# Kernel tuning notes

Hardware: AMD Instinct MI355X
Metric: run time of the kernel (lower is better)

The kernel has to match this reference:

```python
import jax, jax.numpy as jnp
import numpy as np

D_EMB = 64
N_HEADS = 8
D_K = D_EMB // N_HEADS


def setup_inputs() -> dict:
    key = jax.random.key(0)
    ks = jax.random.split(key, 7)
    B, N = 4, 512
    s = 0.02
    return {
        "n": jax.random.normal(ks[0], (B, N, D_EMB), jnp.float32),
        "e": jax.random.normal(ks[1], (B, N, N, D_EMB), jnp.float32),
        # weights stored as (in, out); torch Linear applies x @ W.T
        "W_qkv": jax.random.normal(ks[2], (D_EMB, 3 * D_EMB), jnp.float32) * s,
        "O_n": jax.random.normal(ks[3], (D_EMB, D_EMB), jnp.float32) * s,
        "W_g": jax.random.normal(ks[4], (D_EMB, N_HEADS), jnp.float32) * s,
        "W_e": jax.random.normal(ks[5], (D_EMB, N_HEADS), jnp.float32) * s,
        "O_e": jax.random.normal(ks[6], (N_HEADS, D_EMB), jnp.float32) * s,
    }


def reference(n, e, W_qkv, O_n, W_g, W_e, O_e):
    B, N, _ = n.shape
    H, dk = N_HEADS, D_K
    # QKV projection -> [B, H, N, dk] each
    qkv = (n @ W_qkv).reshape(B, N, 3, H, dk)
    Q = jnp.transpose(qkv[:, :, 0], (0, 2, 1, 3))
    K = jnp.transpose(qkv[:, :, 1], (0, 2, 1, 3))
    V = jnp.transpose(qkv[:, :, 2], (0, 2, 1, 3))
    # per-head edge bias E and gate G: [B, H, N, N]
    E = jnp.transpose(e @ W_e, (0, 3, 1, 2))
    G = jax.nn.sigmoid(jnp.transpose(e @ W_g, (0, 3, 1, 2)))
    dynamic_centrality = jnp.log1p(G.sum(-1))  # [B, H, N]
    # scaled, clamped attention scores plus edge bias
    A_raw = jnp.einsum("bhnd,bhmd->bhnm", Q, K) * (dk ** -0.5)
    A_raw = jnp.clip(A_raw, -5.0, 5.0)
    _E = A_raw + E  # pre-softmax scores, reused for edge output
    A = jax.nn.softmax(_E, axis=-1)
    _V = jnp.einsum("bhnm,bhmd->bhnd", A, V)
    _V = _V * dynamic_centrality[..., None]  # centrality rescale
    n_out = jnp.transpose(_V, (0, 2, 1, 3)).reshape(B, N, H * dk) @ O_n
    e_out = jnp.transpose(_E, (0, 2, 3, 1)) @ O_e  # [B, N, N, d_emb]
    return (n_out, e_out)
```

## Files before the change

kernel.cpp:

```cpp
#include <hip/hip_runtime.h>

#define NN 512
#define SCALE 0.35355339059327373f
#define SMAX 6.0f

typedef short bf16x8 __attribute__((ext_vector_type(8)));
typedef float f32x4 __attribute__((ext_vector_type(4)));

static __device__ __forceinline__ unsigned short bhi16(float x) {
    return (unsigned short)(__float_as_uint(x) >> 16);
}
static __device__ __forceinline__ float btrunc(float x) {
    return __uint_as_float(__float_as_uint(x) & 0xFFFF0000u);
}
static __device__ __forceinline__ unsigned short blo16(float x) {
    return (unsigned short)(__float_as_uint(x - btrunc(x)) >> 16);
}

__global__ __launch_bounds__(64) void qkv_proj(const float* __restrict__ nin,
                                               const float* __restrict__ Wqkv,
                                               float* __restrict__ qkv,
                                               unsigned short* __restrict__ kbf) {
    const int r = blockIdx.x;
    const int j = threadIdx.x;
    const float* nr = nin + (size_t)r * 64;
    float a0 = 0.f, a1 = 0.f, a2 = 0.f;
#pragma unroll
    for (int d = 0; d < 64; ++d) {
        const float nv = nr[d];
        const float* wr = Wqkv + d * 192;
        a0 = fmaf(nv, wr[j], a0);
        a1 = fmaf(nv, wr[64 + j], a1);
        a2 = fmaf(nv, wr[128 + j], a2);
    }
    float* o = qkv + (size_t)r * 192;
    o[j] = a0; o[64 + j] = a1; o[128 + j] = a2;
    kbf[(size_t)r * 64 + j] = bhi16(a1);
}

__device__ __forceinline__ void gload16f(const float* g, float* l) {
    __builtin_amdgcn_global_load_lds(
        (const __attribute__((address_space(1))) unsigned int*)(g),
        (__attribute__((address_space(3))) unsigned int*)(l), 16, 0, 0);
}
__device__ __forceinline__ void gload16u(const unsigned short* g, unsigned short* l) {
    __builtin_amdgcn_global_load_lds(
        (const __attribute__((address_space(1))) unsigned int*)(g),
        (__attribute__((address_space(3))) unsigned int*)(l), 16, 0, 0);
}
#define WAITV(N) asm volatile("s_waitcnt vmcnt(" #N ")" ::: "memory")
#define BARRIER() __builtin_amdgcn_s_barrier()

__global__ __launch_bounds__(256, 2) void edge_mfma5(
    const float* __restrict__ e,
    const float* __restrict__ qkv,
    const unsigned short* __restrict__ kbf,
    const float* __restrict__ We,
    const float* __restrict__ Wg,
    const float* __restrict__ Oe,
    float* __restrict__ e_out,
    float* __restrict__ pvw,
    float* __restrict__ dngs)
{
    __shared__ float ebuf[4][2][16][64];
    __shared__ unsigned short kbl[4][2][16][64];
    __shared__ float Wl[1024];
    __shared__ float Qlds[64];
    __shared__ float Oelds[512];
    __shared__ float E_lds[4][32][8];
    __shared__ float red[256];
    __shared__ float wdn[4][8], wgs[4][8];

    const int t = threadIdx.x, w = t >> 6, l = t & 63;
    const int a2 = l >> 4, m16 = l & 15;
    const int bid = blockIdx.x;
    const int wg = (bid & 7) * 1024 + (bid >> 3);
    const int bn = wg >> 2, chunk = wg & 3;
    const int b = bn >> 9;
    const int rowc = chunk * 128 + w * 32;
    const float* __restrict__ Qp = qkv + (size_t)bn * 192;
    const float* __restrict__ ebase = e + (size_t)bn * 32768;
    float* __restrict__ eob = e_out + (size_t)bn * 32768;

    {
        const float* wsrc = (w < 2) ? (We + w * 256) : (Wg + (w - 2) * 256);
        gload16f(wsrc + l * 4, &Wl[w * 256]);
        if (l < 16) gload16f(Qp + l * 4, &Qlds[0]);
        if (l < 32) gload16f(Oe + w * 128 + l * 4, &Oelds[w * 128]);
    }
#pragma unroll
    for (int s = 0; s < 2; ++s) {
#pragma unroll
        for (int i_ = 0; i_ < 4; ++i_) {
            const int lrow = i_ * 4 + (l >> 4);
            gload16f(ebase + (size_t)(rowc + s * 16 + lrow) * 64 + (((l & 15) ^ lrow) * 4),
                     &ebuf[w][s][i_ * 4][0]);
        }
#pragma unroll
        for (int i_ = 0; i_ < 2; ++i_) {
            const int r8 = i_ * 8 + (l >> 3);
            gload16u(kbf + (size_t)(b * NN + rowc + s * 16 + r8) * 64 + (((l & 7) ^ (r8 & 7)) * 8),
                     &kbl[w][s][i_ * 8][0]);
        }
    }

    WAITV(12);
    BARRIER();

    const int colbase = (m16 < 8) ? m16 : (504 + m16);
    bf16x8 WfB[4], WcB[2], QdB[2];
#pragma unroll
    for (int blk = 0; blk < 4; ++blk) {
#pragma unroll
        for (int jj = 0; jj < 4; ++jj) {
            const int d = blk * 16 + a2 * 4 + jj;
            const short h = (short)bhi16(Wl[d * 8 + colbase]);
            WfB[blk][2 * jj] = h;
            WfB[blk][2 * jj + 1] = h;
        }
    }
#pragma unroll
    for (int c = 0; c < 2; ++c) {
        const int head = c * 4 + a2;
#pragma unroll
        for (int j = 0; j < 8; ++j) {
            const int d = c * 32 + a2 * 8 + j;
            WcB[c][j] = (short)blo16(Wl[d * 8 + colbase]);
            QdB[c][j] = (m16 == head) ? (short)bhi16(Qlds[d]) : (short)0;
        }
    }
    float dn = 0.f, gs = 0.f;

#define SLAB(s, WN) do {                                                         \
        WAITV(WN);                                                               \
        f32x4 c1 = {0.f, 0.f, 0.f, 0.f}, c2 = {0.f, 0.f, 0.f, 0.f};             \
        _Pragma("unroll")                                                        \
        for (int blk = 0; blk < 4; ++blk) {                                      \
            const float4 ev = *(const float4*)&ebuf[w][s][m16]                   \
                                  [(((blk * 4 + a2) ^ m16) * 4)];                \
            bf16x8 af;                                                           \
            af[0] = (short)bhi16(ev.x); af[1] = (short)blo16(ev.x);              \
            af[2] = (short)bhi16(ev.y); af[3] = (short)blo16(ev.y);              \
            af[4] = (short)bhi16(ev.z); af[5] = (short)blo16(ev.z);              \
            af[6] = (short)bhi16(ev.w); af[7] = (short)blo16(ev.w);              \
            c1 = __builtin_amdgcn_mfma_f32_16x16x32_bf16(af, WfB[blk], c1, 0, 0, 0); \
        }                                                                        \
        _Pragma("unroll")                                                        \
        for (int c = 0; c < 2; ++c) {                                            \
            const int g0 = c * 8 + a2 * 2;                                       \
            const float4 e0 = *(const float4*)&ebuf[w][s][m16][((g0 ^ m16) * 4)]; \
            const float4 e1 = *(const float4*)&ebuf[w][s][m16][(((g0 + 1) ^ m16) * 4)]; \
            bf16x8 ac;                                                           \
            ac[0] = (short)bhi16(e0.x); ac[1] = (short)bhi16(e0.y);              \
            ac[2] = (short)bhi16(e0.z); ac[3] = (short)bhi16(e0.w);              \
            ac[4] = (short)bhi16(e1.x); ac[5] = (short)bhi16(e1.y);              \
            ac[6] = (short)bhi16(e1.z); ac[7] = (short)bhi16(e1.w);              \
            c1 = __builtin_amdgcn_mfma_f32_16x16x32_bf16(ac, WcB[c], c1, 0, 0, 0); \
            const bf16x8 kf = *(const bf16x8*)&kbl[w][s][m16]                    \
                                  [(((c * 4 + a2) ^ (m16 & 7)) * 8)];            \
            c2 = __builtin_amdgcn_mfma_f32_16x16x32_bf16(kf, QdB[c], c2, 0, 0, 0); \
        }                                                                        \
        if (m16 < 8) {                                                           \
            _Pragma("unroll")                                                    \
            for (int r = 0; r < 4; ++r) {                                        \
                const float E_ = fminf(fmaxf(c2[r] * SCALE, -5.f), 5.f) + c1[r]; \
                dn += __expf(E_ - SMAX);                                         \
                E_lds[w][(s) * 16 + a2 * 4 + r][m16] = E_;                       \
            }                                                                    \
        } else {                                                                 \
            _Pragma("unroll")                                                    \
            for (int r = 0; r < 4; ++r) gs += 1.f / (1.f + __expf(-c1[r]));      \
        } } while (0)

    SLAB(0, 6);
    SLAB(1, 0);

    dn += __shfl_xor(dn, 16, 64); dn += __shfl_xor(dn, 32, 64);
    gs += __shfl_xor(gs, 16, 64); gs += __shfl_xor(gs, 32, 64);
    if (a2 == 0 && m16 < 8) wdn[w][m16] = dn;
    if (a2 == 0 && m16 >= 8) wgs[w][m16 - 8] = gs;

    {
        const int k = l & 7, hh = (l >> 3) & 7;
        const float* vb = qkv + (size_t)(b * NN + rowc) * 192 + 128 + hh * 8 + k;
        float acc = 0.f;
#pragma unroll 8
        for (int i = 0; i < 32; ++i) {
            const float p = __expf(E_lds[w][i][hh] - SMAX);
            acc = fmaf(p, vb[(size_t)i * 192], acc);
        }
        red[t] = acc;
    }
    __syncthreads();
    if (t < 64)
        pvw[(size_t)wg * 64 + t] = red[t] + red[64 + t] + red[128 + t] + red[192 + t];
    if (t < 8)
        dngs[(size_t)wg * 16 + t] = wdn[0][t] + wdn[1][t] + wdn[2][t] + wdn[3][t];
    else if (t < 16)
        dngs[(size_t)wg * 16 + t] = wgs[0][t - 8] + wgs[1][t - 8] + wgs[2][t - 8] + wgs[3][t - 8];

    {
        const int j4 = l & 15, mr = l >> 4;
        float oc[8][4];
#pragma unroll
        for (int h = 0; h < 8; ++h) {
            const float4 v = *(const float4*)&Oelds[h * 64 + j4 * 4];
            oc[h][0] = v.x; oc[h][1] = v.y; oc[h][2] = v.z; oc[h][3] = v.w;
        }
#pragma unroll 2
        for (int p = 0; p < 8; ++p) {
            const int mloc = p * 4 + mr;
            const float* er = &E_lds[w][mloc][0];
            const float4 ra = *reinterpret_cast<const float4*>(er);
            const float4 rb = *reinterpret_cast<const float4*>(er + 4);
            float o0 = ra.x * oc[0][0], o1 = ra.x * oc[0][1], o2 = ra.x * oc[0][2], o3 = ra.x * oc[0][3];
            o0 = fmaf(ra.y, oc[1][0], o0); o1 = fmaf(ra.y, oc[1][1], o1); o2 = fmaf(ra.y, oc[1][2], o2); o3 = fmaf(ra.y, oc[1][3], o3);
            o0 = fmaf(ra.z, oc[2][0], o0); o1 = fmaf(ra.z, oc[2][1], o1); o2 = fmaf(ra.z, oc[2][2], o2); o3 = fmaf(ra.z, oc[2][3], o3);
            o0 = fmaf(ra.w, oc[3][0], o0); o1 = fmaf(ra.w, oc[3][1], o1); o2 = fmaf(ra.w, oc[3][2], o2); o3 = fmaf(ra.w, oc[3][3], o3);
            o0 = fmaf(rb.x, oc[4][0], o0); o1 = fmaf(rb.x, oc[4][1], o1); o2 = fmaf(rb.x, oc[4][2], o2); o3 = fmaf(rb.x, oc[4][3], o3);
            o0 = fmaf(rb.y, oc[5][0], o0); o1 = fmaf(rb.y, oc[5][1], o1); o2 = fmaf(rb.y, oc[5][2], o2); o3 = fmaf(rb.y, oc[5][3], o3);
            o0 = fmaf(rb.z, oc[6][0], o0); o1 = fmaf(rb.z, oc[6][1], o1); o2 = fmaf(rb.z, oc[6][2], o2); o3 = fmaf(rb.z, oc[6][3], o3);
            o0 = fmaf(rb.w, oc[7][0], o0); o1 = fmaf(rb.w, oc[7][1], o1); o2 = fmaf(rb.w, oc[7][2], o2); o3 = fmaf(rb.w, oc[7][3], o3);
            reinterpret_cast<float4*>(eob + (size_t)(rowc + mloc) * 64 + j4 * 4)[0]
                = make_float4(o0, o1, o2, o3);
        }
    }
#undef SLAB
}

__global__ __launch_bounds__(64) void nout_fin(
    const float* __restrict__ pvw,
    const float* __restrict__ dngs,
    const float* __restrict__ On,
    float* __restrict__ n_out)
{
    __shared__ float vfin[64];
    const int bn = blockIdx.x, t = threadIdx.x;
    const int hh = t >> 3;
    float pv = 0.f, den = 0.f, gsum = 0.f;
#pragma unroll
    for (int c = 0; c < 4; ++c) {
        const size_t wg = (size_t)bn * 4 + c;
        pv += pvw[wg * 64 + t];
        den += dngs[wg * 16 + hh];
        gsum += dngs[wg * 16 + 8 + hh];
    }
    vfin[t] = pv * (1.f / den) * log1pf(gsum);
    __syncthreads();
    float acc = 0.f;
#pragma unroll
    for (int i = 0; i < 64; ++i)
        acc = fmaf(vfin[i], On[i * 64 + t], acc);
    n_out[(size_t)bn * 64 + t] = acc;
}

extern "C" void kernel_launch(void* const* d_in, const int* in_sizes, int n_in,
                              void* d_out, int out_size, void* d_ws, size_t ws_size,
                              hipStream_t stream) {
    const float* n_in_p = (const float*)d_in[0];
    const float* e_p    = (const float*)d_in[1];
    const float* Wqkv   = (const float*)d_in[2];
    const float* On     = (const float*)d_in[3];
    const float* Wg     = (const float*)d_in[4];
    const float* We     = (const float*)d_in[5];
    const float* Oe     = (const float*)d_in[6];
    float* out = (float*)d_out;
    float* n_out = out;
    float* e_out = out + (size_t)4 * 512 * 64;
    float* qkv = (float*)d_ws;
    float* pvw = qkv + 393216;
    float* dngs = pvw + 524288;
    unsigned short* kbf = (unsigned short*)(dngs + 131072);

    hipLaunchKernelGGL(qkv_proj, dim3(4 * NN), dim3(64), 0, stream, n_in_p, Wqkv, qkv, kbf);
    hipLaunchKernelGGL(edge_mfma5, dim3(8192), dim3(256), 0, stream,
                       e_p, qkv, kbf, We, Wg, Oe, e_out, pvw, dngs);
    hipLaunchKernelGGL(nout_fin, dim3(4 * NN), dim3(64), 0, stream,
                       pvw, dngs, On, n_out);
}
```

Before: 176.0 us.

## Single-buffer edge slabs in LDS to raise occupancy to four blocks per CU

Replaces the two-slab LDS prefetch of e and K tiles with a single per-wave buffer, issuing the second slab's loads only after the first slab is computed. Roughly halving the LDS footprint allows launch bounds to request four resident blocks instead of two. The aim is to hide memory latency through more concurrent workgroups rather than intra-block prefetch. In exchange, each block now serialises its two slab loads behind compute. There is also a possible read-after-reuse hazard when async loads overwrite the buffer just read.

```diff
diff --git a/kernel.cpp b/kernel.cpp
--- a/kernel.cpp
+++ b/kernel.cpp
@@ -51,7 +51,7 @@
 #define WAITV(N) asm volatile("s_waitcnt vmcnt(" #N ")" ::: "memory")
 #define BARRIER() __builtin_amdgcn_s_barrier()
 
-__global__ __launch_bounds__(256, 2) void edge_mfma5(
+__global__ __launch_bounds__(256, 4) void edge_mfma6(
     const float* __restrict__ e,
     const float* __restrict__ qkv,
     const unsigned short* __restrict__ kbf,
@@ -62,8 +62,8 @@
     float* __restrict__ pvw,
     float* __restrict__ dngs)
 {
-    __shared__ float ebuf[4][2][16][64];
-    __shared__ unsigned short kbl[4][2][16][64];
+    __shared__ float ebuf[4][16][64];
+    __shared__ unsigned short kbl[4][16][64];
     __shared__ float Wl[1024];
     __shared__ float Qlds[64];
     __shared__ float Oelds[512];
@@ -82,29 +82,30 @@
     const float* __restrict__ ebase = e + (size_t)bn * 32768;
     float* __restrict__ eob = e_out + (size_t)bn * 32768;
 
+#define STAGE_E(s) do {                                                          \
+        _Pragma("unroll")                                                        \
+        for (int i_ = 0; i_ < 4; ++i_) {                                         \
+            const int lrow = i_ * 4 + (l >> 4);                                  \
+            gload16f(ebase + (size_t)(rowc + (s) * 16 + lrow) * 64 + (((l & 15) ^ lrow) * 4), \
+                     &ebuf[w][i_ * 4][0]);                                       \
+        } } while (0)
+#define STAGE_K(s) do {                                                          \
+        _Pragma("unroll")                                                        \
+        for (int i_ = 0; i_ < 2; ++i_) {                                         \
+            const int r8 = i_ * 8 + (l >> 3);                                    \
+            gload16u(kbf + (size_t)(b * NN + rowc + (s) * 16 + r8) * 64 + (((l & 7) ^ (r8 & 7)) * 8), \
+                     &kbl[w][i_ * 8][0]);                                        \
+        } } while (0)
+
     {
         const float* wsrc = (w < 2) ? (We + w * 256) : (Wg + (w - 2) * 256);
         gload16f(wsrc + l * 4, &Wl[w * 256]);
         if (l < 16) gload16f(Qp + l * 4, &Qlds[0]);
         if (l < 32) gload16f(Oe + w * 128 + l * 4, &Oelds[w * 128]);
     }
-#pragma unroll
-    for (int s = 0; s < 2; ++s) {
-#pragma unroll
-        for (int i_ = 0; i_ < 4; ++i_) {
-            const int lrow = i_ * 4 + (l >> 4);
-            gload16f(ebase + (size_t)(rowc + s * 16 + lrow) * 64 + (((l & 15) ^ lrow) * 4),
-                     &ebuf[w][s][i_ * 4][0]);
-        }
-#pragma unroll
-        for (int i_ = 0; i_ < 2; ++i_) {
-            const int r8 = i_ * 8 + (l >> 3);
-            gload16u(kbf + (size_t)(b * NN + rowc + s * 16 + r8) * 64 + (((l & 7) ^ (r8 & 7)) * 8),
-                     &kbl[w][s][i_ * 8][0]);
-        }
-    }
-
-    WAITV(12);
+    STAGE_E(0); STAGE_K(0);
+
+    WAITV(6);
     BARRIER();
 
     const int colbase = (m16 < 8) ? m16 : (504 + m16);
@@ -131,12 +132,11 @@
     }
     float dn = 0.f, gs = 0.f;
 
-#define SLAB(s, WN) do {                                                         \
-        WAITV(WN);                                                               \
+#define SLAB(s) do {                                                             \
         f32x4 c1 = {0.f, 0.f, 0.f, 0.f}, c2 = {0.f, 0.f, 0.f, 0.f};             \
         _Pragma("unroll")                                                        \
         for (int blk = 0; blk < 4; ++blk) {                                      \
-            const float4 ev = *(const float4*)&ebuf[w][s][m16]                   \
+            const float4 ev = *(const float4*)&ebuf[w][m16]                      \
                                   [(((blk * 4 + a2) ^ m16) * 4)];                \
             bf16x8 af;                                                           \
             af[0] = (short)bhi16(ev.x); af[1] = (short)blo16(ev.x);              \
@@ -148,15 +148,15 @@
         _Pragma("unroll")                                                        \
         for (int c = 0; c < 2; ++c) {                                            \
             const int g0 = c * 8 + a2 * 2;                                       \
-            const float4 e0 = *(const float4*)&ebuf[w][s][m16][((g0 ^ m16) * 4)]; \
-            const float4 e1 = *(const float4*)&ebuf[w][s][m16][(((g0 + 1) ^ m16) * 4)]; \
+            const float4 e0 = *(const float4*)&ebuf[w][m16][((g0 ^ m16) * 4)];   \
+            const float4 e1 = *(const float4*)&ebuf[w][m16][(((g0 + 1) ^ m16) * 4)]; \
             bf16x8 ac;                                                           \
             ac[0] = (short)bhi16(e0.x); ac[1] = (short)bhi16(e0.y);              \
             ac[2] = (short)bhi16(e0.z); ac[3] = (short)bhi16(e0.w);              \
             ac[4] = (short)bhi16(e1.x); ac[5] = (short)bhi16(e1.y);              \
             ac[6] = (short)bhi16(e1.z); ac[7] = (short)bhi16(e1.w);              \
             c1 = __builtin_amdgcn_mfma_f32_16x16x32_bf16(ac, WcB[c], c1, 0, 0, 0); \
-            const bf16x8 kf = *(const bf16x8*)&kbl[w][s][m16]                    \
+            const bf16x8 kf = *(const bf16x8*)&kbl[w][m16]                       \
                                   [(((c * 4 + a2) ^ (m16 & 7)) * 8)];            \
             c2 = __builtin_amdgcn_mfma_f32_16x16x32_bf16(kf, QdB[c], c2, 0, 0, 0); \
         }                                                                        \
@@ -172,8 +172,11 @@
             for (int r = 0; r < 4; ++r) gs += 1.f / (1.f + __expf(-c1[r]));      \
         } } while (0)
 
-    SLAB(0, 6);
-    SLAB(1, 0);
+    WAITV(0);
+    SLAB(0);
+    STAGE_E(1); STAGE_K(1);
+    WAITV(0);
+    SLAB(1);
 
     dn += __shfl_xor(dn, 16, 64); dn += __shfl_xor(dn, 32, 64);
     gs += __shfl_xor(gs, 16, 64); gs += __shfl_xor(gs, 32, 64);
@@ -225,6 +228,8 @@
                 = make_float4(o0, o1, o2, o3);
         }
     }
+#undef STAGE_E
+#undef STAGE_K
 #undef SLAB
 }
 
@@ -273,7 +278,7 @@
     unsigned short* kbf = (unsigned short*)(dngs + 131072);
 
     hipLaunchKernelGGL(qkv_proj, dim3(4 * NN), dim3(64), 0, stream, n_in_p, Wqkv, qkv, kbf);
-    hipLaunchKernelGGL(edge_mfma5, dim3(8192), dim3(256), 0, stream,
+    hipLaunchKernelGGL(edge_mfma6, dim3(8192), dim3(256), 0, stream,
                        e_p, qkv, kbf, We, Wg, Oe, e_out, pvw, dngs);
     hipLaunchKernelGGL(nout_fin, dim3(4 * NN), dim3(64), 0, stream,
                        pvw, dngs, On, n_out);
```

Result: faster. 158.1 us (-10.2%).
